# Optimization experiments

Hardware: AMD Instinct MI355X
Metric: run time of the kernel (lower is better)

The kernel has to match this reference:

```python
import jax, jax.numpy as jnp
import numpy as np
from jax.scipy.linalg import solve_triangular

B, T, HID = 1, 2048, 2048
HK, DK = 16, 96
HV, DV = 16, 192
KDIM, VDIM = HK * DK, HV * DV
KCONV = 4
CHUNK = 64
EPS = 1e-6


def setup_inputs():
    key = jax.random.key(0)
    ks = jax.random.split(key, 16)
    s = 0.02
    return {
        "hidden_states": jax.random.normal(ks[0], (B, T, HID), jnp.float32),
        "Wq": jax.random.normal(ks[1], (HID, KDIM), jnp.float32) * s,
        "Wk": jax.random.normal(ks[2], (HID, KDIM), jnp.float32) * s,
        "Wv": jax.random.normal(ks[3], (HID, VDIM), jnp.float32) * s,
        "Wb": jax.random.normal(ks[4], (HID, HV), jnp.float32) * s,
        "Wa": jax.random.normal(ks[5], (HID, HV), jnp.float32) * s,
        "Wg": jax.random.normal(ks[6], (HID, VDIM), jnp.float32) * s,
        "Wo": jax.random.normal(ks[7], (VDIM, HID), jnp.float32) * s,
        "conv_q": jax.random.normal(ks[8], (KDIM, KCONV), jnp.float32) * 0.5,
        "conv_k": jax.random.normal(ks[9], (KDIM, KCONV), jnp.float32) * 0.5,
        "conv_v": jax.random.normal(ks[10], (VDIM, KCONV), jnp.float32) * 0.5,
        "A_log": jnp.log(jax.random.uniform(ks[11], (HV,), jnp.float32, 1.0, 16.0)),
        "dt_bias": jax.random.uniform(ks[12], (HV,), jnp.float32, 0.0, 1.0),
        "norm_weight": jnp.ones((DV,), jnp.float32),
    }


def short_conv_silu(x, w):
    # x: [B,T,C], w: [C,K]; causal depthwise conv (left pad K-1) then SiLU
    K = w.shape[-1]
    xp = jnp.pad(x, ((0, 0), (K - 1, 0), (0, 0)))
    y = sum(xp[:, j:j + x.shape[1], :] * w[:, j] for j in range(K))
    return jax.nn.silu(y)


def l2norm(x):
    return x * jax.lax.rsqrt(jnp.sum(x * x, axis=-1, keepdims=True) + EPS)


def chunk_gated_delta_rule(q, k, v, g, beta):
    # q,k: [B,T,H,dk]; v: [B,T,H,dv]; g,beta: [B,T,H]. Chunked parallel scan (WY form).
    Bb, Tt, H, dk = q.shape
    dv = v.shape[-1]
    N = Tt // CHUNK
    q = l2norm(q) * (dk ** -0.5)
    k = l2norm(k)
    chunk = lambda x: x.transpose(0, 2, 1, 3).reshape(Bb, H, N, CHUNK, x.shape[-1])
    qc, kc, vc = chunk(q), chunk(k), chunk(v)
    gc = jnp.cumsum(g.transpose(0, 2, 1).reshape(Bb, H, N, CHUNK), axis=-1)
    bc = beta.transpose(0, 2, 1).reshape(Bb, H, N, CHUNK)

    m_inc = jnp.tril(jnp.ones((CHUNK, CHUNK), bool))
    m_str = jnp.tril(jnp.ones((CHUNK, CHUNK), bool), -1)
    diff = gc[..., :, None] - gc[..., None, :]
    D = jnp.exp(jnp.where(m_inc, diff, 0.0)) * m_inc  # [B,H,N,C,C] intra-chunk decay

    kb = kc * bc[..., None]
    A = -jnp.einsum('bhnik,bhnjk->bhnij', kb, kc) * D * m_str
    eye = jnp.eye(CHUNK, dtype=q.dtype)
    # UT transform: Tm = (I - A)^{-1}, A strictly lower triangular
    Tm = solve_triangular(eye - A, jnp.broadcast_to(eye, A.shape), lower=True, unit_diagonal=True)
    u = Tm @ (vc * bc[..., None])                   # [B,H,N,C,dv]
    w = Tm @ (kb * jnp.exp(gc)[..., None])          # [B,H,N,C,dk]
    g_last = gc[..., -1]                            # [B,H,N]

    def step(S, inp):
        q_i, k_i, u_i, w_i, g_i, D_i, gl = inp
        v_new = u_i - w_i @ S                       # [B,H,C,dv]
        attn = jnp.einsum('bhik,bhjk->bhij', q_i, k_i) * D_i
        o_i = (q_i * jnp.exp(g_i)[..., None]) @ S + attn @ v_new
        k_dec = k_i * jnp.exp(gl[..., None] - g_i)[..., None]
        S = S * jnp.exp(gl)[..., None, None] + jnp.einsum('bhck,bhcv->bhkv', k_dec, v_new)
        return S, o_i

    mv = lambda x: jnp.moveaxis(x, 2, 0)
    S0 = jnp.zeros((Bb, H, dk, dv), q.dtype)
    _, o = jax.lax.scan(step, S0, (mv(qc), mv(kc), mv(u), mv(w), mv(gc), mv(D), mv(g_last)))
    o = jnp.moveaxis(o, 0, 2).reshape(Bb, H, Tt, dv)
    return o.transpose(0, 2, 1, 3)                  # [B,T,H,dv]


def reference(hidden_states, Wq, Wk, Wv, Wb, Wa, Wg, Wo, conv_q, conv_k, conv_v, A_log, dt_bias, norm_weight):
    q = short_conv_silu(hidden_states @ Wq, conv_q).reshape(B, T, HK, DK)
    k = short_conv_silu(hidden_states @ Wk, conv_k).reshape(B, T, HK, DK)
    v = short_conv_silu(hidden_states @ Wv, conv_v).reshape(B, T, HV, DV)
    beta = jax.nn.sigmoid(hidden_states @ Wb) * 2.0          # allow_neg_eigval -> beta in [0,2]
    g = -jnp.exp(A_log) * jax.nn.softplus(hidden_states @ Wa + dt_bias)  # log decay, [B,T,HV]
    o = chunk_gated_delta_rule(q, k, v, g, beta)             # [B,T,HV,DV]
    gate = (hidden_states @ Wg).reshape(B, T, HV, DV)
    o = o * jax.nn.silu(gate)                                # gated RMSNorm (gate, then norm)
    o = o * jax.lax.rsqrt(jnp.mean(o * o, axis=-1, keepdims=True) + EPS) * norm_weight
    return o.reshape(B, T, VDIM) @ Wo
```

## Files before the change

kernel.cpp:

```cpp
#include <hip/hip_runtime.h>
#include <math.h>

#define T_LEN 2048
#define HIDN  2048
#define HKN   16
#define DKN   96
#define HVN   16
#define DVN   192
#define KDIMN 1536
#define VDIMN 3072
#define QKVD  6144
#define CHUNKN 64
#define NCHUNK 32
#define EPSF 1e-6f
#define TN_STRIDE 10240
#define WQG_ST 6656
#define AT_ST  4608
#define CT_ST  18432
#define S_ST   19968
#define U_ST   12288

typedef __attribute__((ext_vector_type(8))) short short8;
typedef __attribute__((ext_vector_type(4))) float f32x4;

__device__ __forceinline__ unsigned short f2bf(float f) {
    unsigned int u = __float_as_uint(f);
    unsigned int r = (u + 0x7FFFu + ((u >> 16) & 1u)) >> 16;
    return (unsigned short)r;
}
__device__ __forceinline__ float bf2f(unsigned short u) {
    return __uint_as_float(((unsigned int)u) << 16);
}
__device__ __forceinline__ float siluf(float x) { return x / (1.f + expf(-x)); }

__device__ __forceinline__ void gld_lds16(const void* g, void* l) {
    __builtin_amdgcn_global_load_lds((const __attribute__((address_space(1))) unsigned int*)g,
                                     (__attribute__((address_space(3))) unsigned int*)l, 16, 0, 0);
}

__global__ void prep_weights(const float* __restrict__ Wq, const float* __restrict__ Wk,
                             const float* __restrict__ Wv, const float* __restrict__ Wg,
                             const float* __restrict__ Wo,
                             unsigned short* __restrict__ WallT, unsigned short* __restrict__ WoT) {
    __shared__ float tile[64][65];
    int bid = blockIdx.x;
    const float* W; unsigned short* Wt; int K, N, l;
    if (bid < 768)       { W = Wq; Wt = WallT;                          K = 2048; N = 1536; l = bid; }
    else if (bid < 1536) { W = Wk; Wt = WallT + (size_t)1536 * 2048;    K = 2048; N = 1536; l = bid - 768; }
    else if (bid < 3072) { W = Wv; Wt = WallT + (size_t)3072 * 2048;    K = 2048; N = 3072; l = bid - 1536; }
    else if (bid < 4608) { W = Wg; Wt = WallT + (size_t)6144 * 2048;    K = 2048; N = 3072; l = bid - 3072; }
    else                 { W = Wo; Wt = WoT;                            K = 3072; N = 2048; l = bid - 4608; }
    int nbx = N >> 6;
    int n0 = (l % nbx) * 64, k0 = (l / nbx) * 64;
    int tx = threadIdx.x, ty = threadIdx.y;
    for (int r = ty; r < 64; r += 4) tile[r][tx] = W[(size_t)(k0 + r) * N + n0 + tx];
    __syncthreads();
    for (int r = ty; r < 64; r += 4) Wt[(size_t)(n0 + r) * K + k0 + tx] = f2bf(tile[tx][r]);
}

__global__ __launch_bounds__(256) void gemm_bt2(const unsigned short* __restrict__ A,
                                                const unsigned short* __restrict__ Bt,
                                                float* __restrict__ C1, int ld1, int nblk1,
                                                unsigned short* __restrict__ C2, int ld2,
                                                int M, int K) {
    __shared__ __align__(16) unsigned short As[2][128 * 32];
    __shared__ __align__(16) unsigned short Bs[2][128 * 32];
    int tid = threadIdx.x;
    int wave = tid >> 6, lane = tid & 63;
    int bm = blockIdx.y, bn = blockIdx.x;
    f32x4 acc[4][4] = {};
    int wr = wave >> 1, wc = wave & 1;
    int rstage = wave * 32 + (lane >> 2);
    int cstage = (lane & 3) * 8;
    const size_t a_row0 = (size_t)bm * 128;
    const size_t b_row0 = (size_t)bn * 128;
    const unsigned short* gaBase = A + (a_row0 + rstage) * (size_t)K + cstage;
    const unsigned short* gbBase = Bt + (b_row0 + rstage) * (size_t)K + cstage;
    int row_a[4], row_b[4];
#pragma unroll
    for (int i = 0; i < 4; ++i) {
        row_a[i] = wr * 64 + i * 16 + (lane & 15);
        row_b[i] = wc * 64 + i * 16 + (lane & 15);
    }
    int koff = (lane >> 4) * 8;
    int niter = K >> 5;
    {
        unsigned short* ab = &As[0][wave * 1024];
        unsigned short* bb = &Bs[0][wave * 1024];
        gld_lds16(gaBase, ab);
        gld_lds16(gaBase + (size_t)16 * K, ab + 512);
        gld_lds16(gbBase, bb);
        gld_lds16(gbBase + (size_t)16 * K, bb + 512);
    }
    __syncthreads();
    for (int i = 0; i < niter; ++i) {
        int cur = i & 1;
        if (i + 1 < niter) {
            int k0 = (i + 1) * 32;
            unsigned short* ab = &As[cur ^ 1][wave * 1024];
            unsigned short* bb = &Bs[cur ^ 1][wave * 1024];
            gld_lds16(gaBase + k0, ab);
            gld_lds16(gaBase + k0 + (size_t)16 * K, ab + 512);
            gld_lds16(gbBase + k0, bb);
            gld_lds16(gbBase + k0 + (size_t)16 * K, bb + 512);
        }
        short8 af[4], bfr[4];
#pragma unroll
        for (int mi = 0; mi < 4; ++mi) af[mi] = *(const short8*)&As[cur][row_a[mi] * 32 + koff];
#pragma unroll
        for (int ni = 0; ni < 4; ++ni) bfr[ni] = *(const short8*)&Bs[cur][row_b[ni] * 32 + koff];
#pragma unroll
        for (int mi = 0; mi < 4; ++mi)
#pragma unroll
            for (int ni = 0; ni < 4; ++ni)
                acc[mi][ni] = __builtin_amdgcn_mfma_f32_16x16x32_bf16(af[mi], bfr[ni], acc[mi][ni], 0, 0, 0);
        __syncthreads();
    }
    if (bn < nblk1) {
        int colb = bn * 128;
#pragma unroll
        for (int mi = 0; mi < 4; ++mi) {
            int rbase = bm * 128 + wr * 64 + mi * 16 + (lane >> 4) * 4;
#pragma unroll
            for (int ni = 0; ni < 4; ++ni) {
                int col = colb + wc * 64 + ni * 16 + (lane & 15);
#pragma unroll
                for (int j = 0; j < 4; ++j)
                    C1[(size_t)(rbase + j) * ld1 + col] = acc[mi][ni][j];
            }
        }
    } else {
        int colb = (bn - nblk1) * 128;
#pragma unroll
        for (int mi = 0; mi < 4; ++mi) {
            int rbase = bm * 128 + wr * 64 + mi * 16 + (lane >> 4) * 4;
#pragma unroll
            for (int ni = 0; ni < 4; ++ni) {
                int col = colb + wc * 64 + ni * 16 + (lane & 15);
#pragma unroll
                for (int j = 0; j < 4; ++j)
                    C2[(size_t)(rbase + j) * ld2 + col] = f2bf(acc[mi][ni][j]);
            }
        }
    }
}

__global__ __launch_bounds__(256) void gemm_btk(const unsigned short* __restrict__ A,
                                                const unsigned short* __restrict__ Bt,
                                                float* __restrict__ C, float* __restrict__ Cp,
                                                int M, int N, int K) {
    __shared__ __align__(16) unsigned short As[2][128 * 32];
    __shared__ __align__(16) unsigned short Bs[2][128 * 32];
    int tid = threadIdx.x;
    int wave = tid >> 6, lane = tid & 63;
    int bm = blockIdx.y, bn = blockIdx.x, kz = blockIdx.z;
    int kchunk = K / 3;
    int kbeg = kz * kchunk;
    f32x4 acc[4][4] = {};
    int wr = wave >> 1, wc = wave & 1;
    int rstage = wave * 32 + (lane >> 2);
    int cstage = (lane & 3) * 8;
    const size_t a_row0 = (size_t)bm * 128;
    const size_t b_row0 = (size_t)bn * 128;
    const unsigned short* gaBase = A + (a_row0 + rstage) * (size_t)K + kbeg + cstage;
    const unsigned short* gbBase = Bt + (b_row0 + rstage) * (size_t)K + kbeg + cstage;
    int row_a[4], row_b[4];
#pragma unroll
    for (int i = 0; i < 4; ++i) {
        row_a[i] = wr * 64 + i * 16 + (lane & 15);
        row_b[i] = wc * 64 + i * 16 + (lane & 15);
    }
    int koff = (lane >> 4) * 8;
    int niter = kchunk >> 5;
    {
        unsigned short* ab = &As[0][wave * 1024];
        unsigned short* bb = &Bs[0][wave * 1024];
        gld_lds16(gaBase, ab);
        gld_lds16(gaBase + (size_t)16 * K, ab + 512);
        gld_lds16(gbBase, bb);
        gld_lds16(gbBase + (size_t)16 * K, bb + 512);
    }
    __syncthreads();
    for (int i = 0; i < niter; ++i) {
        int cur = i & 1;
        if (i + 1 < niter) {
            int k0 = (i + 1) * 32;
            unsigned short* ab = &As[cur ^ 1][wave * 1024];
            unsigned short* bb = &Bs[cur ^ 1][wave * 1024];
            gld_lds16(gaBase + k0, ab);
            gld_lds16(gaBase + k0 + (size_t)16 * K, ab + 512);
            gld_lds16(gbBase + k0, bb);
            gld_lds16(gbBase + k0 + (size_t)16 * K, bb + 512);
        }
        short8 af[4], bfr[4];
#pragma unroll
        for (int mi = 0; mi < 4; ++mi) af[mi] = *(const short8*)&As[cur][row_a[mi] * 32 + koff];
#pragma unroll
        for (int ni = 0; ni < 4; ++ni) bfr[ni] = *(const short8*)&Bs[cur][row_b[ni] * 32 + koff];
#pragma unroll
        for (int mi = 0; mi < 4; ++mi)
#pragma unroll
            for (int ni = 0; ni < 4; ++ni)
                acc[mi][ni] = __builtin_amdgcn_mfma_f32_16x16x32_bf16(af[mi], bfr[ni], acc[mi][ni], 0, 0, 0);
        __syncthreads();
    }
    float* Cout = (kz == 0) ? C : (Cp + (size_t)(kz - 1) * M * N);
#pragma unroll
    for (int mi = 0; mi < 4; ++mi) {
        int rbase = bm * 128 + wr * 64 + mi * 16 + (lane >> 4) * 4;
#pragma unroll
        for (int ni = 0; ni < 4; ++ni) {
            int col = bn * 128 + wc * 64 + ni * 16 + (lane & 15);
#pragma unroll
            for (int j = 0; j < 4; ++j)
                Cout[(size_t)(rbase + j) * N + col] = acc[mi][ni][j];
        }
    }
}

__global__ void addk(float* __restrict__ out, const float* __restrict__ p, int n) {
    int i = (blockIdx.x * blockDim.x + threadIdx.x) * 4;
    if (i >= n) return;
    float4 a = *(const float4*)(out + i);
    float4 b = *(const float4*)(p + i);
    float4 c = *(const float4*)(p + n + i);
    a.x += b.x + c.x; a.y += b.y + c.y; a.z += b.z + c.z; a.w += b.w + c.w;
    *(float4*)(out + i) = a;
}

__global__ __launch_bounds__(256) void beta_g(const float* __restrict__ X,
                                              const float* __restrict__ Wb, const float* __restrict__ Wa,
                                              const float* __restrict__ A_log, const float* __restrict__ dtb,
                                              float* __restrict__ bvec, float* __restrict__ gvec,
                                              unsigned short* __restrict__ Xbf) {
    int t = blockIdx.x;
    int tid = threadIdx.x;
    int cg = tid & 7, ks = tid >> 3;
    int wave = tid >> 6, lane = tid & 63;
    const float* xr = X + (size_t)t * HIDN;
    const float* Wsel = (cg < 4) ? Wb : Wa;
    int cc = (cg & 3) * 4;
    float ax = 0.f, ay = 0.f, az = 0.f, aw = 0.f;
#pragma unroll 4
    for (int i = 0; i < 16; ++i) {
        int k = (ks + 32 * i) * 4;
        float4 xv = *(const float4*)(xr + k);
        if (cg == 0) {
            ushort4 xo;
            xo.x = f2bf(xv.x); xo.y = f2bf(xv.y); xo.z = f2bf(xv.z); xo.w = f2bf(xv.w);
            *(ushort4*)(Xbf + (size_t)t * HIDN + k) = xo;
        }
        float4 w0 = *(const float4*)(Wsel + (size_t)(k + 0) * 16 + cc);
        float4 w1 = *(const float4*)(Wsel + (size_t)(k + 1) * 16 + cc);
        float4 w2 = *(const float4*)(Wsel + (size_t)(k + 2) * 16 + cc);
        float4 w3 = *(const float4*)(Wsel + (size_t)(k + 3) * 16 + cc);
        ax += xv.x * w0.x + xv.y * w1.x + xv.z * w2.x + xv.w * w3.x;
        ay += xv.x * w0.y + xv.y * w1.y + xv.z * w2.y + xv.w * w3.y;
        az += xv.x * w0.z + xv.y * w1.z + xv.z * w2.z + xv.w * w3.z;
        aw += xv.x * w0.w + xv.y * w1.w + xv.z * w2.w + xv.w * w3.w;
    }
#pragma unroll
    for (int off = 8; off <= 32; off <<= 1) {
        ax += __shfl_xor(ax, off, 64);
        ay += __shfl_xor(ay, off, 64);
        az += __shfl_xor(az, off, 64);
        aw += __shfl_xor(aw, off, 64);
    }
    __shared__ float red[4][8][4];
    if ((lane >> 3) == 0) {
        red[wave][cg][0] = ax; red[wave][cg][1] = ay;
        red[wave][cg][2] = az; red[wave][cg][3] = aw;
    }
    __syncthreads();
    if (tid < 8) {
        float tot[4];
#pragma unroll
        for (int j = 0; j < 4; ++j)
            tot[j] = red[0][tid][j] + red[1][tid][j] + red[2][tid][j] + red[3][tid][j];
        int c0 = (tid & 3) * 4;
        if (tid < 4) {
#pragma unroll
            for (int j = 0; j < 4; ++j)
                bvec[(size_t)t * 16 + c0 + j] = 2.f / (1.f + expf(-tot[j]));
        } else {
#pragma unroll
            for (int j = 0; j < 4; ++j) {
                float a = tot[j] + dtb[c0 + j];
                float sp = (a > 20.f) ? a : log1pf(expf(a));
                gvec[(size_t)t * 16 + c0 + j] = -expf(A_log[c0 + j]) * sp;
            }
        }
    }
}

__global__ __launch_bounds__(256) void phase1_mfma(
    const float* __restrict__ Cqkv,
    const float* __restrict__ cq, const float* __restrict__ ck, const float* __restrict__ cv,
    const float* __restrict__ gvec, const float* __restrict__ bvec,
    float* __restrict__ u_ws, unsigned short* __restrict__ w_bf,
    unsigned short* __restrict__ qg_bf, unsigned short* __restrict__ at_bf,
    unsigned short* __restrict__ Ct, unsigned short* __restrict__ Tn) {
    int n = blockIdx.x, h = blockIdx.y;
    int t0 = n * CHUNKN;
    int tid = threadIdx.x;
    int wave = tid >> 6, lane = tid & 63;
    size_t base = (size_t)(h * NCHUNK + n);

    __shared__ __align__(16) char LB1[139776];
    unsigned short* QKb  = (unsigned short*)(LB1 + 0);
    unsigned short* Pb   = (unsigned short*)(LB1 + 26624);
    unsigned short* RHSw = (unsigned short*)(LB1 + 39936);
    unsigned short* RHSv = (unsigned short*)(LB1 + 53760);
    unsigned short* Ab   = (unsigned short*)(LB1 + 81408);
    unsigned short* Atb  = (unsigned short*)(LB1 + 94720);
    unsigned short* Ptb  = (unsigned short*)(LB1 + 108032);
    float*          Pf   = (float*)(LB1 + 121344);
    unsigned short* kdT  = (unsigned short*)(LB1 + 81408);
    unsigned short* wT   = (unsigned short*)(LB1 + 95232);
    unsigned short* uT   = (unsigned short*)(LB1 + 109056);
    float* gr_s = (float*)(LB1 + 138752);
    float* gc_s = gr_s + 64;
    float* be_s = gc_s + 64;
    float* egc  = be_s + 64;
    __shared__ __align__(16) float cwS[384 * 4];

    for (int f = tid; f < 384; f += 256) {
        const float* src = (f < 96)  ? (cq + (size_t)(h * 96 + f) * 4)
                         : (f < 192) ? (ck + (size_t)(h * 96 + f - 96) * 4)
                                     : (cv + (size_t)(h * 192 + f - 192) * 4);
        *(float4*)&cwS[f * 4] = *(const float4*)src;
    }
    if (tid < 64) {
        gr_s[tid] = gvec[(size_t)(t0 + tid) * HVN + h];
        be_s[tid] = bvec[(size_t)(t0 + tid) * HVN + h];
    }
    __syncthreads();
    if (tid < 64) {
        float sacc = 0.f;
        for (int j = 0; j <= tid; ++j) sacc += gr_s[j];
        gc_s[tid] = sacc;
    }
    __syncthreads();
    float gl = gc_s[63];
    if (tid < 64) egc[tid] = expf(gl - gc_s[tid]);

    int r = tid >> 2, sub = tid & 3;
    int trow = t0 + r;
    {
        int gc0 = 1536 + h * DKN + sub * 24;
        int lc0 = 96 + sub * 24;
        float kreg[24];
        float ss = 0.f;
#pragma unroll
        for (int i = 0; i < 6; ++i) {
            float4 x0 = (trow >= 3) ? *(const float4*)(Cqkv + (size_t)(trow - 3) * QKVD + gc0 + i * 4) : make_float4(0, 0, 0, 0);
            float4 x1 = (trow >= 2) ? *(const float4*)(Cqkv + (size_t)(trow - 2) * QKVD + gc0 + i * 4) : make_float4(0, 0, 0, 0);
            float4 x2 = (trow >= 1) ? *(const float4*)(Cqkv + (size_t)(trow - 1) * QKVD + gc0 + i * 4) : make_float4(0, 0, 0, 0);
            float4 x3 = *(const float4*)(Cqkv + (size_t)trow * QKVD + gc0 + i * 4);
#pragma unroll
            for (int c = 0; c < 4; ++c) {
                float4 w = *(const float4*)&cwS[(lc0 + i * 4 + c) * 4];
                float xv = ((const float*)&x0)[c] * w.x + ((const float*)&x1)[c] * w.y
                         + ((const float*)&x2)[c] * w.z + ((const float*)&x3)[c] * w.w;
                xv = siluf(xv);
                kreg[i * 4 + c] = xv;
                ss += xv * xv;
            }
        }
        ss += __shfl_xor(ss, 1, 64);
        ss += __shfl_xor(ss, 2, 64);
        float nrm = rsqrtf(ss + EPSF);
        float ebg = be_s[r] * expf(gc_s[r]);
#pragma unroll
        for (int i = 0; i < 24; ++i) {
            float kn = kreg[i] * nrm;
            QKb[r * 104 + sub * 24 + i] = f2bf(kn);
            RHSw[(sub * 24 + i) * 72 + r] = f2bf(kn * ebg);
        }
    }
    {
        int gc0 = h * DKN + sub * 24;
        int lc0 = sub * 24;
        float qreg[24];
        float ss = 0.f;
#pragma unroll
        for (int i = 0; i < 6; ++i) {
            float4 x0 = (trow >= 3) ? *(const float4*)(Cqkv + (size_t)(trow - 3) * QKVD + gc0 + i * 4) : make_float4(0, 0, 0, 0);
            float4 x1 = (trow >= 2) ? *(const float4*)(Cqkv + (size_t)(trow - 2) * QKVD + gc0 + i * 4) : make_float4(0, 0, 0, 0);
            float4 x2 = (trow >= 1) ? *(const float4*)(Cqkv + (size_t)(trow - 1) * QKVD + gc0 + i * 4) : make_float4(0, 0, 0, 0);
            float4 x3 = *(const float4*)(Cqkv + (size_t)trow * QKVD + gc0 + i * 4);
#pragma unroll
            for (int c = 0; c < 4; ++c) {
                float4 w = *(const float4*)&cwS[(lc0 + i * 4 + c) * 4];
                float xv = ((const float*)&x0)[c] * w.x + ((const float*)&x1)[c] * w.y
                         + ((const float*)&x2)[c] * w.z + ((const float*)&x3)[c] * w.w;
                xv = siluf(xv);
                qreg[i * 4 + c] = xv;
                ss += xv * xv;
            }
        }
        ss += __shfl_xor(ss, 1, 64);
        ss += __shfl_xor(ss, 2, 64);
        float nrm = rsqrtf(ss + EPSF) * 0.10206207261596577f;
        float eg = expf(gc_s[r]);
        unsigned short* qgp = qg_bf + base * WQG_ST + r * 104 + sub * 24;
#pragma unroll
        for (int i = 0; i < 24; ++i) {
            float qn = qreg[i] * nrm;
            QKb[(64 + r) * 104 + sub * 24 + i] = f2bf(qn);
            qgp[i] = f2bf(qn * eg);
        }
    }
    {
        int gc0 = 3072 + h * DVN + sub * 48;
        int lc0 = 192 + sub * 48;
        float ber = be_s[r];
#pragma unroll
        for (int i = 0; i < 12; ++i) {
            float4 x0 = (trow >= 3) ? *(const float4*)(Cqkv + (size_t)(trow - 3) * QKVD + gc0 + i * 4) : make_float4(0, 0, 0, 0);
            float4 x1 = (trow >= 2) ? *(const float4*)(Cqkv + (size_t)(trow - 2) * QKVD + gc0 + i * 4) : make_float4(0, 0, 0, 0);
            float4 x2 = (trow >= 1) ? *(const float4*)(Cqkv + (size_t)(trow - 1) * QKVD + gc0 + i * 4) : make_float4(0, 0, 0, 0);
            float4 x3 = *(const float4*)(Cqkv + (size_t)trow * QKVD + gc0 + i * 4);
#pragma unroll
            for (int c = 0; c < 4; ++c) {
                float4 w = *(const float4*)&cwS[(lc0 + i * 4 + c) * 4];
                float xv = ((const float*)&x0)[c] * w.x + ((const float*)&x1)[c] * w.y
                         + ((const float*)&x2)[c] * w.z + ((const float*)&x3)[c] * w.w;
                RHSv[(sub * 48 + i * 4 + c) * 72 + r] = f2bf(siluf(xv) * ber);
            }
        }
    }
    __syncthreads();

    {
        f32x4 acc1[2][4] = {};
#pragma unroll
        for (int ks = 0; ks < 3; ++ks) {
            int ko = ks * 32 + (lane >> 4) * 8;
            short8 af[2], bfv[4];
#pragma unroll
            for (int rt2 = 0; rt2 < 2; ++rt2)
                af[rt2] = *(const short8*)&QKb[(wave * 32 + rt2 * 16 + (lane & 15)) * 104 + ko];
#pragma unroll
            for (int ct = 0; ct < 4; ++ct)
                bfv[ct] = *(const short8*)&QKb[(ct * 16 + (lane & 15)) * 104 + ko];
#pragma unroll
            for (int rt2 = 0; rt2 < 2; ++rt2)
#pragma unroll
                for (int ct = 0; ct < 4; ++ct)
                    acc1[rt2][ct] = __builtin_amdgcn_mfma_f32_16x16x32_bf16(af[rt2], bfv[ct], acc1[rt2][ct], 0, 0, 0);
        }
#pragma unroll
        for (int rt2 = 0; rt2 < 2; ++rt2)
#pragma unroll
            for (int ct = 0; ct < 4; ++ct)
#pragma unroll
                for (int j = 0; j < 4; ++j) {
                    int rr = wave * 32 + rt2 * 16 + (lane >> 4) * 4 + j;
                    int cc = ct * 16 + (lane & 15);
                    float val = acc1[rt2][ct][j];
                    if (rr < 64) {
                        float av = (rr > cc) ? -be_s[rr] * expf(gc_s[rr] - gc_s[cc]) * val : 0.f;
                        unsigned short ab = f2bf(av);
                        Ab[rr * 104 + cc] = ab;
                        Atb[cc * 104 + rr] = ab;
                        float pv = (rr == cc) ? 1.f : av;
                        Pf[rr * 68 + cc] = pv;
                        unsigned short pb = f2bf(pv);
                        Pb[rr * 104 + cc] = pb;
                        Ptb[cc * 104 + rr] = pb;
                    } else {
                        int ar = rr - 64;
                        float av = (ar >= cc) ? expf(gc_s[ar] - gc_s[cc]) * val : 0.f;
                        at_bf[base * AT_ST + ar * 72 + cc] = f2bf(av);
                    }
                }
    }
    __syncthreads();

#pragma unroll 1
    for (int lev = 0; lev < 5; ++lev) {
        f32x4 d[4] = {};
#pragma unroll
        for (int ks = 0; ks < 2; ++ks) {
            int ko = ks * 32 + (lane >> 4) * 8;
            short8 a0 = *(const short8*)&Ab[(wave * 16 + (lane & 15)) * 104 + ko];
#pragma unroll
            for (int ct = 0; ct < 4; ++ct) {
                short8 b0 = *(const short8*)&Atb[(ct * 16 + (lane & 15)) * 104 + ko];
                d[ct] = __builtin_amdgcn_mfma_f32_16x16x32_bf16(a0, b0, d[ct], 0, 0, 0);
            }
        }
        __syncthreads();
#pragma unroll
        for (int ct = 0; ct < 4; ++ct)
#pragma unroll
            for (int j = 0; j < 4; ++j) {
                int rr = wave * 16 + (lane >> 4) * 4 + j;
                int cc = ct * 16 + (lane & 15);
                unsigned short hb = f2bf(d[ct][j]);
                Ab[rr * 104 + cc] = hb;
                Atb[cc * 104 + rr] = hb;
            }
        __syncthreads();
        f32x4 e[4];
#pragma unroll
        for (int ct = 0; ct < 4; ++ct)
#pragma unroll
            for (int j = 0; j < 4; ++j)
                e[ct][j] = Pf[(wave * 16 + (lane >> 4) * 4 + j) * 68 + ct * 16 + (lane & 15)];
#pragma unroll
        for (int ks = 0; ks < 2; ++ks) {
            int ko = ks * 32 + (lane >> 4) * 8;
            short8 a0 = *(const short8*)&Ab[(wave * 16 + (lane & 15)) * 104 + ko];
#pragma unroll
            for (int ct = 0; ct < 4; ++ct) {
                short8 b0 = *(const short8*)&Ptb[(ct * 16 + (lane & 15)) * 104 + ko];
                e[ct] = __builtin_amdgcn_mfma_f32_16x16x32_bf16(a0, b0, e[ct], 0, 0, 0);
            }
        }
        __syncthreads();
#pragma unroll
        for (int ct = 0; ct < 4; ++ct)
#pragma unroll
            for (int j = 0; j < 4; ++j) {
                int rr = wave * 16 + (lane >> 4) * 4 + j;
                int cc = ct * 16 + (lane & 15);
                float pv = e[ct][j];
                Pf[rr * 68 + cc] = pv;
                unsigned short pb = f2bf(pv);
                Pb[rr * 104 + cc] = pb;
                Ptb[cc * 104 + rr] = pb;
            }
        __syncthreads();
    }
    for (int f = tid; f < 6144; f += 256) {
        int d = f >> 6, tt = f & 63;
        kdT[d * 72 + tt] = f2bf(bf2f(QKb[tt * 104 + d]) * egc[tt]);
    }

#pragma unroll 1
    for (int i = 0; i < 18; ++i) {
        int id = wave * 18 + i;
        int rt = id & 3, ct = id >> 2;
        f32x4 o4 = {};
#pragma unroll
        for (int ks = 0; ks < 2; ++ks) {
            int ko = ks * 32 + (lane >> 4) * 8;
            short8 a0 = *(const short8*)&Pb[(rt * 16 + (lane & 15)) * 104 + ko];
            short8 b0 = (ct < 12)
                ? *(const short8*)&RHSv[(ct * 16 + (lane & 15)) * 72 + ko]
                : *(const short8*)&RHSw[((ct - 12) * 16 + (lane & 15)) * 72 + ko];
            o4 = __builtin_amdgcn_mfma_f32_16x16x32_bf16(a0, b0, o4, 0, 0, 0);
        }
#pragma unroll
        for (int j = 0; j < 4; ++j) {
            int rr = rt * 16 + (lane >> 4) * 4 + j;
            int nn = ct * 16 + (lane & 15);
            if (ct < 12) {
                u_ws[base * U_ST + rr * 192 + nn] = o4[j];
                uT[nn * 72 + rr] = f2bf(o4[j]);
            } else {
                w_bf[base * WQG_ST + rr * 104 + (nn - 192)] = f2bf(-o4[j]);
                wT[(nn - 192) * 72 + rr] = f2bf(o4[j]);
            }
        }
    }
    __syncthreads();

    float eglv = expf(gl);
#pragma unroll 1
    for (int q = 0; q < 27; ++q) {
        int id = wave * 27 + q;
        f32x4 acc = {};
        if (id < 36) {
            int jt = id / 6, kt = id % 6;
#pragma unroll
            for (int ks = 0; ks < 2; ++ks) {
                int ko = ks * 32 + (lane >> 4) * 8;
                short8 a0 = *(const short8*)&kdT[(jt * 16 + (lane & 15)) * 72 + ko];
                short8 b0 = *(const short8*)&wT[(kt * 16 + (lane & 15)) * 72 + ko];
                acc = __builtin_amdgcn_mfma_f32_16x16x32_bf16(a0, b0, acc, 0, 0, 0);
            }
#pragma unroll
            for (int rr = 0; rr < 4; ++rr) {
                int j = jt * 16 + (lane >> 4) * 4 + rr;
                int k = kt * 16 + (lane & 15);
                float val = -acc[rr];
                if (j == k) val += eglv;
                Tn[base * TN_STRIDE + j * 104 + k] = f2bf(val);
            }
        } else {
            int cid = id - 36;
            int it = cid / 6, jt = cid % 6;
#pragma unroll
            for (int ks = 0; ks < 2; ++ks) {
                int ko = ks * 32 + (lane >> 4) * 8;
                short8 a0 = *(const short8*)&uT[(it * 16 + (lane & 15)) * 72 + ko];
                short8 b0 = *(const short8*)&kdT[(jt * 16 + (lane & 15)) * 72 + ko];
                acc = __builtin_amdgcn_mfma_f32_16x16x32_bf16(a0, b0, acc, 0, 0, 0);
            }
#pragma unroll
            for (int rr = 0; rr < 4; ++rr)
                Ct[base * CT_ST + (size_t)(it * 16 + (lane >> 4) * 4 + rr) * 96 + jt * 16 + (lane & 15)] = f2bf(acc[rr]);
        }
    }
}

__global__ __launch_bounds__(128) void mscan(const unsigned short* __restrict__ Ct,
                                             const unsigned short* __restrict__ Tn,
                                             unsigned short* __restrict__ s_bf) {
    int rg = blockIdx.x, h = blockIdx.y;
    int tid = threadIdx.x, wave = tid >> 6, lane = tid & 63;
    __shared__ __align__(16) unsigned short St[48 * 104];
    __shared__ __align__(16) unsigned short TnB[2][TN_STRIDE];
    __shared__ __align__(16) unsigned short CtB[2][48 * 96];
    for (int i = tid; i < 48 * 104; i += 128) St[i] = 0;

    {
        const char* cp = (const char*)(Ct + (size_t)(h * NCHUNK) * CT_ST + rg * (48 * 96));
        const char* tp = (const char*)(Tn + (size_t)(h * NCHUNK) * TN_STRIDE);
        for (int q = wave; q < 9; q += 2)
            gld_lds16(cp + (size_t)q * 1024 + lane * 16, (char*)&CtB[0][0] + (size_t)q * 1024);
#pragma unroll
        for (int q = 0; q < 10; ++q) {
            size_t o = (size_t)(wave * 10 + q) * 1024 + lane * 16;
            gld_lds16(tp + o, (char*)&TnB[0][0] + (size_t)(wave * 10 + q) * 1024);
        }
    }
    f32x4 acc[3][3];
    int colw = wave * 48;
    __syncthreads();

#pragma unroll 1
    for (int n = 0; n < NCHUNK; ++n) {
        size_t base = (size_t)(h * NCHUNK + n);
        int cur = n & 1;
        if (n + 1 < NCHUNK) {
            const char* cp = (const char*)(Ct + (base + 1) * CT_ST + rg * (48 * 96));
            const char* tp = (const char*)(Tn + (base + 1) * TN_STRIDE);
            for (int q = wave; q < 9; q += 2)
                gld_lds16(cp + (size_t)q * 1024 + lane * 16, (char*)&CtB[cur ^ 1][0] + (size_t)q * 1024);
#pragma unroll
            for (int q = 0; q < 10; ++q) {
                size_t o = (size_t)(wave * 10 + q) * 1024 + lane * 16;
                gld_lds16(tp + o, (char*)&TnB[cur ^ 1][0] + (size_t)(wave * 10 + q) * 1024);
            }
        }
        {
            unsigned short* sp = s_bf + base * S_ST + rg * 4992;
            for (int f = tid; f < 624; f += 128)
                *(short8*)(sp + f * 8) = *(const short8*)&St[f * 8];
        }
#pragma unroll
        for (int it = 0; it < 3; ++it)
#pragma unroll
            for (int jt = 0; jt < 3; ++jt) {
                int irow = it * 16 + (lane >> 4) * 4;
                int col = colw + jt * 16 + (lane & 15);
#pragma unroll
                for (int r = 0; r < 4; ++r)
                    acc[it][jt][r] = bf2f(CtB[cur][(irow + r) * 96 + col]);
            }
#pragma unroll
        for (int ks = 0; ks < 3; ++ks) {
            int ko = ks * 32 + (lane >> 4) * 8;
            short8 af[3], bfv[3];
#pragma unroll
            for (int it = 0; it < 3; ++it)
                af[it] = *(const short8*)&St[(it * 16 + (lane & 15)) * 104 + ko];
#pragma unroll
            for (int jt = 0; jt < 3; ++jt)
                bfv[jt] = *(const short8*)&TnB[cur][(colw + jt * 16 + (lane & 15)) * 104 + ko];
#pragma unroll
            for (int it = 0; it < 3; ++it)
#pragma unroll
                for (int jt = 0; jt < 3; ++jt)
                    acc[it][jt] = __builtin_amdgcn_mfma_f32_16x16x32_bf16(af[it], bfv[jt], acc[it][jt], 0, 0, 0);
        }
        __syncthreads();
#pragma unroll
        for (int it = 0; it < 3; ++it)
#pragma unroll
            for (int jt = 0; jt < 3; ++jt)
#pragma unroll
                for (int r = 0; r < 4; ++r)
                    St[(it * 16 + (lane >> 4) * 4 + r) * 104 + colw + jt * 16 + (lane & 15)] = f2bf(acc[it][jt][r]);
        __syncthreads();
    }
}

#define P2_ST 0
#define P2_W  39936
#define P2_QG 53248
#define P2_AT 66560
#define P2_U  75776
#define P2_VN 125952
__global__ __launch_bounds__(256) void phase2b_mfma(const unsigned short* __restrict__ s_bf,
                                                    const unsigned short* __restrict__ w_bf,
                                                    const unsigned short* __restrict__ qg_bf,
                                                    const unsigned short* __restrict__ at_bf,
                                                    const float* __restrict__ u_ws,
                                                    const unsigned short* __restrict__ Cgate,
                                                    const float* __restrict__ nw,
                                                    unsigned short* __restrict__ obf) {
    __shared__ __align__(16) char LB[153600];
    unsigned short* StB = (unsigned short*)(LB + P2_ST);
    unsigned short* wB  = (unsigned short*)(LB + P2_W);
    unsigned short* qgB = (unsigned short*)(LB + P2_QG);
    unsigned short* atB = (unsigned short*)(LB + P2_AT);
    float* uF           = (float*)(LB + P2_U);
    unsigned short* vnB = (unsigned short*)(LB + P2_VN);
    int n = blockIdx.x, h = blockIdx.y;
    size_t base = (size_t)(h * NCHUNK + n);
    int tid = threadIdx.x, wave = tid >> 6, lane = tid & 63;
    int i0w = wave * 48;
    {
        const char* sp = (const char*)(s_bf + base * S_ST);
        const char* wp = (const char*)(w_bf + base * WQG_ST);
        const char* qp = (const char*)(qg_bf + base * WQG_ST);
        const char* ap = (const char*)(at_bf + base * AT_ST);
        for (int q = wave; q < 39; q += 4)
            gld_lds16(sp + (size_t)q * 1024 + lane * 16, LB + P2_ST + (size_t)q * 1024);
        for (int q = wave; q < 13; q += 4)
            gld_lds16(wp + (size_t)q * 1024 + lane * 16, LB + P2_W + (size_t)q * 1024);
        for (int q = wave; q < 13; q += 4)
            gld_lds16(qp + (size_t)q * 1024 + lane * 16, LB + P2_QG + (size_t)q * 1024);
        for (int q = wave; q < 9; q += 4)
            gld_lds16(ap + (size_t)q * 1024 + lane * 16, LB + P2_AT + (size_t)q * 1024);
    }
    {
        const float* up = u_ws + base * U_ST;
        for (int f = tid; f < 3072; f += 256) {
            int t = f / 48, c4 = (f % 48) * 4;
            *(float4*)&uF[t * 196 + c4] = *(const float4*)(up + t * 192 + c4);
        }
    }
    __syncthreads();
    {
        f32x4 acc[3][4];
#pragma unroll
        for (int it = 0; it < 3; ++it)
#pragma unroll
            for (int jt = 0; jt < 4; ++jt)
#pragma unroll
                for (int r = 0; r < 4; ++r)
                    acc[it][jt][r] = uF[(jt * 16 + (lane & 15)) * 196 + i0w + it * 16 + (lane >> 4) * 4 + r];
#pragma unroll
        for (int ks = 0; ks < 3; ++ks) {
            int ko = ks * 32 + (lane >> 4) * 8;
            short8 af[3], bfv[4];
#pragma unroll
            for (int it = 0; it < 3; ++it)
                af[it] = *(const short8*)&StB[(i0w + it * 16 + (lane & 15)) * 104 + ko];
#pragma unroll
            for (int jt = 0; jt < 4; ++jt)
                bfv[jt] = *(const short8*)&wB[(jt * 16 + (lane & 15)) * 104 + ko];
#pragma unroll
            for (int it = 0; it < 3; ++it)
#pragma unroll
                for (int jt = 0; jt < 4; ++jt)
                    acc[it][jt] = __builtin_amdgcn_mfma_f32_16x16x32_bf16(af[it], bfv[jt], acc[it][jt], 0, 0, 0);
        }
#pragma unroll
        for (int it = 0; it < 3; ++it)
#pragma unroll
            for (int jt = 0; jt < 4; ++jt)
#pragma unroll
                for (int r = 0; r < 4; ++r)
                    vnB[(i0w + it * 16 + (lane >> 4) * 4 + r) * 72 + jt * 16 + (lane & 15)] = f2bf(acc[it][jt][r]);
    }
    f32x4 acc2[3][4] = {};
#pragma unroll
    for (int ks = 0; ks < 3; ++ks) {
        int ko = ks * 32 + (lane >> 4) * 8;
        short8 af[3], bfv[4];
#pragma unroll
        for (int it = 0; it < 3; ++it)
            af[it] = *(const short8*)&StB[(i0w + it * 16 + (lane & 15)) * 104 + ko];
#pragma unroll
        for (int jt = 0; jt < 4; ++jt)
            bfv[jt] = *(const short8*)&qgB[(jt * 16 + (lane & 15)) * 104 + ko];
#pragma unroll
        for (int it = 0; it < 3; ++it)
#pragma unroll
            for (int jt = 0; jt < 4; ++jt)
                acc2[it][jt] = __builtin_amdgcn_mfma_f32_16x16x32_bf16(af[it], bfv[jt], acc2[it][jt], 0, 0, 0);
    }
#pragma unroll
    for (int ks = 0; ks < 2; ++ks) {
        int ko = ks * 32 + (lane >> 4) * 8;
        short8 af[3], bfv[4];
#pragma unroll
        for (int it = 0; it < 3; ++it)
            af[it] = *(const short8*)&vnB[(i0w + it * 16 + (lane & 15)) * 72 + ko];
#pragma unroll
        for (int jt = 0; jt < 4; ++jt)
            bfv[jt] = *(const short8*)&atB[(jt * 16 + (lane & 15)) * 72 + ko];
#pragma unroll
        for (int it = 0; it < 3; ++it)
#pragma unroll
            for (int jt = 0; jt < 4; ++jt)
                acc2[it][jt] = __builtin_amdgcn_mfma_f32_16x16x32_bf16(af[it], bfv[jt], acc2[it][jt], 0, 0, 0);
    }
    __syncthreads();
    float* oF = (float*)(LB + 0);
#pragma unroll
    for (int it = 0; it < 3; ++it)
#pragma unroll
        for (int jt = 0; jt < 4; ++jt)
#pragma unroll
            for (int r = 0; r < 4; ++r)
                oF[(i0w + it * 16 + (lane >> 4) * 4 + r) * 68 + jt * 16 + (lane & 15)] = acc2[it][jt][r];
    __syncthreads();

    float* ssq = (float*)(LB + 131072);
    float* rno = (float*)(LB + 132096);
    int jj = tid >> 2, qq = tid & 3;
    int t0 = n * CHUNKN;
    {
        const unsigned short* gp = Cgate + (size_t)(t0 + jj) * VDIMN + h * DVN + qq * 48;
        float ss = 0.f;
#pragma unroll 4
        for (int m = 0; m < 48; ++m) {
            int i = qq * 48 + m;
            float x = oF[i * 68 + jj];
            float g = bf2f(gp[m]);
            float xv = x * siluf(g);
            oF[i * 68 + jj] = xv;
            ss += xv * xv;
        }
        ssq[jj * 4 + qq] = ss;
    }
    __syncthreads();
    if (tid < 64) {
        float tot = ssq[tid * 4] + ssq[tid * 4 + 1] + ssq[tid * 4 + 2] + ssq[tid * 4 + 3];
        rno[tid] = rsqrtf(tot * (1.f / 192.f) + EPSF);
    }
    __syncthreads();
    {
        float rr2 = rno[jj];
        unsigned short* op = obf + (size_t)(t0 + jj) * VDIMN + h * DVN + qq * 48;
#pragma unroll 4
        for (int m = 0; m < 48; ++m) {
            int i = qq * 48 + m;
            op[m] = f2bf(oF[i * 68 + jj] * rr2 * nw[i]);
        }
    }
}

extern "C" void kernel_launch(void* const* d_in, const int* in_sizes, int n_in,
                              void* d_out, int out_size, void* d_ws, size_t ws_size,
                              hipStream_t stream) {
    (void)in_sizes; (void)n_in; (void)out_size;
    const float* X    = (const float*)d_in[0];
    const float* Wq   = (const float*)d_in[1];
    const float* Wk   = (const float*)d_in[2];
    const float* Wv   = (const float*)d_in[3];
    const float* Wb   = (const float*)d_in[4];
    const float* Wa   = (const float*)d_in[5];
    const float* Wg   = (const float*)d_in[6];
    const float* Wo   = (const float*)d_in[7];
    const float* cq   = (const float*)d_in[8];
    const float* ck   = (const float*)d_in[9];
    const float* cv   = (const float*)d_in[10];
    const float* Alog = (const float*)d_in[11];
    const float* dtb  = (const float*)d_in[12];
    const float* nw   = (const float*)d_in[13];

    const size_t OFF_XBF   = 0;
    const size_t OFF_WALLT = 8388608;
    const size_t OFF_WOT   = 46137344;
    const size_t OFF_CQKV  = 58720256;
    const size_t OFF_CGATE = 109051904;
    const size_t OFF_CT    = 134217728;
    const size_t OFF_TN    = OFF_CT + 37748736;
    const size_t OFF_GVEC  = 184549376;
    const size_t OFF_BVEC  = 184680448;
    const size_t OFF_U     = 184819712;
    const size_t OFF_W     = 209985536;
    const size_t OFF_QG    = 222568448;
    const size_t OFF_AT    = OFF_XBF;
    const size_t OFF_S     = OFF_CQKV;
    const size_t OFF_OBF   = OFF_WALLT + 25165824;
    const size_t OFF_OPART = OFF_CQKV;
    const size_t NEEDED    = 235151360;
    if (ws_size < NEEDED) return;

    char* ws = (char*)d_ws;
    unsigned short* Xbf   = (unsigned short*)(ws + OFF_XBF);
    unsigned short* WallT = (unsigned short*)(ws + OFF_WALLT);
    unsigned short* WoT   = (unsigned short*)(ws + OFF_WOT);
    float* Cqkv  = (float*)(ws + OFF_CQKV);
    unsigned short* Cgate = (unsigned short*)(ws + OFF_CGATE);
    float* gvec  = (float*)(ws + OFF_GVEC);
    float* bvec  = (float*)(ws + OFF_BVEC);
    float* u_ws  = (float*)(ws + OFF_U);
    unsigned short* w_bf  = (unsigned short*)(ws + OFF_W);
    unsigned short* qg_bf = (unsigned short*)(ws + OFF_QG);
    unsigned short* at_bf = (unsigned short*)(ws + OFF_AT);
    unsigned short* Ct    = (unsigned short*)(ws + OFF_CT);
    unsigned short* Tn    = (unsigned short*)(ws + OFF_TN);
    unsigned short* s_bf  = (unsigned short*)(ws + OFF_S);
    unsigned short* obf   = (unsigned short*)(ws + OFF_OBF);
    float* opart = (float*)(ws + OFF_OPART);

    beta_g<<<T_LEN, 256, 0, stream>>>(X, Wb, Wa, Alog, dtb, bvec, gvec, Xbf);
    prep_weights<<<6144, dim3(64, 4), 0, stream>>>(Wq, Wk, Wv, Wg, Wo, WallT, WoT);

    gemm_bt2<<<dim3(9216 / 128, 2048 / 128), 256, 0, stream>>>(Xbf, WallT,
                                                               Cqkv, QKVD, QKVD / 128,
                                                               Cgate, VDIMN, 2048, 2048);

    phase1_mfma<<<dim3(NCHUNK, HVN), 256, 0, stream>>>(Cqkv, cq, ck, cv, gvec, bvec,
                                                       u_ws, w_bf, qg_bf, at_bf, Ct, Tn);
    mscan<<<dim3(4, HVN), 128, 0, stream>>>(Ct, Tn, s_bf);
    phase2b_mfma<<<dim3(NCHUNK, HVN), 256, 0, stream>>>(s_bf, w_bf, qg_bf, at_bf, u_ws,
                                                        Cgate, nw, obf);

    gemm_btk<<<dim3(2048 / 128, 2048 / 128, 3), 256, 0, stream>>>(obf, WoT, (float*)d_out, opart,
                                                                  2048, 2048, 3072);
    addk<<<4096, 256, 0, stream>>>((float*)d_out, opart, 2048 * 2048);
}
```

Before: 402.7 us.

## Merge prep kernels and restructure triangular inverse doubling to one sync phase per level

Fuses the beta/g projection kernel and the weight transpose/convert kernel into one launch, removing a kernel launch boundary. In phase1, the product-form inverse (I+A)(I+A^2)... is rewritten so that each level computes both the next power of A and the accumulated product P from the same operands in one pass. This removes one barrier pair and the transposed P buffer per level, at the cost of one extra level of the product MMA. The merged prep kernel shares an LDS footprint and launch config between two different workloads.

```diff
diff --git a/kernel.cpp b/kernel.cpp
--- a/kernel.cpp
+++ b/kernel.cpp
@@ -38,24 +38,91 @@
                                      (__attribute__((address_space(3))) unsigned int*)l, 16, 0, 0);
 }
 
-__global__ void prep_weights(const float* __restrict__ Wq, const float* __restrict__ Wk,
-                             const float* __restrict__ Wv, const float* __restrict__ Wg,
-                             const float* __restrict__ Wo,
-                             unsigned short* __restrict__ WallT, unsigned short* __restrict__ WoT) {
+__global__ __launch_bounds__(256) void prep_all(
+    const float* __restrict__ X,
+    const float* __restrict__ Wb, const float* __restrict__ Wa,
+    const float* __restrict__ A_log, const float* __restrict__ dtb,
+    float* __restrict__ bvec, float* __restrict__ gvec, unsigned short* __restrict__ Xbf,
+    const float* __restrict__ Wq, const float* __restrict__ Wk,
+    const float* __restrict__ Wv, const float* __restrict__ Wg,
+    const float* __restrict__ Wo,
+    unsigned short* __restrict__ WallT, unsigned short* __restrict__ WoT) {
     __shared__ float tile[64][65];
+    __shared__ float red[4][8][4];
     int bid = blockIdx.x;
-    const float* W; unsigned short* Wt; int K, N, l;
-    if (bid < 768)       { W = Wq; Wt = WallT;                          K = 2048; N = 1536; l = bid; }
-    else if (bid < 1536) { W = Wk; Wt = WallT + (size_t)1536 * 2048;    K = 2048; N = 1536; l = bid - 768; }
-    else if (bid < 3072) { W = Wv; Wt = WallT + (size_t)3072 * 2048;    K = 2048; N = 3072; l = bid - 1536; }
-    else if (bid < 4608) { W = Wg; Wt = WallT + (size_t)6144 * 2048;    K = 2048; N = 3072; l = bid - 3072; }
-    else                 { W = Wo; Wt = WoT;                            K = 3072; N = 2048; l = bid - 4608; }
-    int nbx = N >> 6;
-    int n0 = (l % nbx) * 64, k0 = (l / nbx) * 64;
-    int tx = threadIdx.x, ty = threadIdx.y;
-    for (int r = ty; r < 64; r += 4) tile[r][tx] = W[(size_t)(k0 + r) * N + n0 + tx];
-    __syncthreads();
-    for (int r = ty; r < 64; r += 4) Wt[(size_t)(n0 + r) * K + k0 + tx] = f2bf(tile[tx][r]);
+    int tid = threadIdx.x;
+    if (bid < 2048) {
+        int t = bid;
+        int cg = tid & 7, ks = tid >> 3;
+        int wave = tid >> 6, lane = tid & 63;
+        const float* xr = X + (size_t)t * HIDN;
+        const float* Wsel = (cg < 4) ? Wb : Wa;
+        int cc = (cg & 3) * 4;
+        float ax = 0.f, ay = 0.f, az = 0.f, aw = 0.f;
+#pragma unroll 4
+        for (int i = 0; i < 16; ++i) {
+            int k = (ks + 32 * i) * 4;
+            float4 xv = *(const float4*)(xr + k);
+            if (cg == 0) {
+                ushort4 xo;
+                xo.x = f2bf(xv.x); xo.y = f2bf(xv.y); xo.z = f2bf(xv.z); xo.w = f2bf(xv.w);
+                *(ushort4*)(Xbf + (size_t)t * HIDN + k) = xo;
+            }
+            float4 w0 = *(const float4*)(Wsel + (size_t)(k + 0) * 16 + cc);
+            float4 w1 = *(const float4*)(Wsel + (size_t)(k + 1) * 16 + cc);
+            float4 w2 = *(const float4*)(Wsel + (size_t)(k + 2) * 16 + cc);
+            float4 w3 = *(const float4*)(Wsel + (size_t)(k + 3) * 16 + cc);
+            ax += xv.x * w0.x + xv.y * w1.x + xv.z * w2.x + xv.w * w3.x;
+            ay += xv.x * w0.y + xv.y * w1.y + xv.z * w2.y + xv.w * w3.y;
+            az += xv.x * w0.z + xv.y * w1.z + xv.z * w2.z + xv.w * w3.z;
+            aw += xv.x * w0.w + xv.y * w1.w + xv.z * w2.w + xv.w * w3.w;
+        }
+#pragma unroll
+        for (int off = 8; off <= 32; off <<= 1) {
+            ax += __shfl_xor(ax, off, 64);
+            ay += __shfl_xor(ay, off, 64);
+            az += __shfl_xor(az, off, 64);
+            aw += __shfl_xor(aw, off, 64);
+        }
+        if ((lane >> 3) == 0) {
+            red[wave][cg][0] = ax; red[wave][cg][1] = ay;
+            red[wave][cg][2] = az; red[wave][cg][3] = aw;
+        }
+        __syncthreads();
+        if (tid < 8) {
+            float tot[4];
+#pragma unroll
+            for (int j = 0; j < 4; ++j)
+                tot[j] = red[0][tid][j] + red[1][tid][j] + red[2][tid][j] + red[3][tid][j];
+            int c0 = (tid & 3) * 4;
+            if (tid < 4) {
+#pragma unroll
+                for (int j = 0; j < 4; ++j)
+                    bvec[(size_t)t * 16 + c0 + j] = 2.f / (1.f + expf(-tot[j]));
+            } else {
+#pragma unroll
+                for (int j = 0; j < 4; ++j) {
+                    float a = tot[j] + dtb[c0 + j];
+                    float sp = (a > 20.f) ? a : log1pf(expf(a));
+                    gvec[(size_t)t * 16 + c0 + j] = -expf(A_log[c0 + j]) * sp;
+                }
+            }
+        }
+    } else {
+        int b2 = bid - 2048;
+        const float* W; unsigned short* Wt; int K, N, l;
+        if (b2 < 768)       { W = Wq; Wt = WallT;                       K = 2048; N = 1536; l = b2; }
+        else if (b2 < 1536) { W = Wk; Wt = WallT + (size_t)1536 * 2048; K = 2048; N = 1536; l = b2 - 768; }
+        else if (b2 < 3072) { W = Wv; Wt = WallT + (size_t)3072 * 2048; K = 2048; N = 3072; l = b2 - 1536; }
+        else if (b2 < 4608) { W = Wg; Wt = WallT + (size_t)6144 * 2048; K = 2048; N = 3072; l = b2 - 3072; }
+        else                { W = Wo; Wt = WoT;                         K = 3072; N = 2048; l = b2 - 4608; }
+        int nbx = N >> 6;
+        int n0 = (l % nbx) * 64, k0 = (l / nbx) * 64;
+        int tx = tid & 63, ty = tid >> 6;
+        for (int r = ty; r < 64; r += 4) tile[r][tx] = W[(size_t)(k0 + r) * N + n0 + tx];
+        __syncthreads();
+        for (int r = ty; r < 64; r += 4) Wt[(size_t)(n0 + r) * K + k0 + tx] = f2bf(tile[tx][r]);
+    }
 }
 
 __global__ __launch_bounds__(256) void gemm_bt2(const unsigned short* __restrict__ A,
@@ -228,71 +295,6 @@
     *(float4*)(out + i) = a;
 }
 
-__global__ __launch_bounds__(256) void beta_g(const float* __restrict__ X,
-                                              const float* __restrict__ Wb, const float* __restrict__ Wa,
-                                              const float* __restrict__ A_log, const float* __restrict__ dtb,
-                                              float* __restrict__ bvec, float* __restrict__ gvec,
-                                              unsigned short* __restrict__ Xbf) {
-    int t = blockIdx.x;
-    int tid = threadIdx.x;
-    int cg = tid & 7, ks = tid >> 3;
-    int wave = tid >> 6, lane = tid & 63;
-    const float* xr = X + (size_t)t * HIDN;
-    const float* Wsel = (cg < 4) ? Wb : Wa;
-    int cc = (cg & 3) * 4;
-    float ax = 0.f, ay = 0.f, az = 0.f, aw = 0.f;
-#pragma unroll 4
-    for (int i = 0; i < 16; ++i) {
-        int k = (ks + 32 * i) * 4;
-        float4 xv = *(const float4*)(xr + k);
-        if (cg == 0) {
-            ushort4 xo;
-            xo.x = f2bf(xv.x); xo.y = f2bf(xv.y); xo.z = f2bf(xv.z); xo.w = f2bf(xv.w);
-            *(ushort4*)(Xbf + (size_t)t * HIDN + k) = xo;
-        }
-        float4 w0 = *(const float4*)(Wsel + (size_t)(k + 0) * 16 + cc);
-        float4 w1 = *(const float4*)(Wsel + (size_t)(k + 1) * 16 + cc);
-        float4 w2 = *(const float4*)(Wsel + (size_t)(k + 2) * 16 + cc);
-        float4 w3 = *(const float4*)(Wsel + (size_t)(k + 3) * 16 + cc);
-        ax += xv.x * w0.x + xv.y * w1.x + xv.z * w2.x + xv.w * w3.x;
-        ay += xv.x * w0.y + xv.y * w1.y + xv.z * w2.y + xv.w * w3.y;
-        az += xv.x * w0.z + xv.y * w1.z + xv.z * w2.z + xv.w * w3.z;
-        aw += xv.x * w0.w + xv.y * w1.w + xv.z * w2.w + xv.w * w3.w;
-    }
-#pragma unroll
-    for (int off = 8; off <= 32; off <<= 1) {
-        ax += __shfl_xor(ax, off, 64);
-        ay += __shfl_xor(ay, off, 64);
-        az += __shfl_xor(az, off, 64);
-        aw += __shfl_xor(aw, off, 64);
-    }
-    __shared__ float red[4][8][4];
-    if ((lane >> 3) == 0) {
-        red[wave][cg][0] = ax; red[wave][cg][1] = ay;
-        red[wave][cg][2] = az; red[wave][cg][3] = aw;
-    }
-    __syncthreads();
-    if (tid < 8) {
-        float tot[4];
-#pragma unroll
-        for (int j = 0; j < 4; ++j)
-            tot[j] = red[0][tid][j] + red[1][tid][j] + red[2][tid][j] + red[3][tid][j];
-        int c0 = (tid & 3) * 4;
-        if (tid < 4) {
-#pragma unroll
-            for (int j = 0; j < 4; ++j)
-                bvec[(size_t)t * 16 + c0 + j] = 2.f / (1.f + expf(-tot[j]));
-        } else {
-#pragma unroll
-            for (int j = 0; j < 4; ++j) {
-                float a = tot[j] + dtb[c0 + j];
-                float sp = (a > 20.f) ? a : log1pf(expf(a));
-                gvec[(size_t)t * 16 + c0 + j] = -expf(A_log[c0 + j]) * sp;
-            }
-        }
-    }
-}
-
 __global__ __launch_bounds__(256) void phase1_mfma(
     const float* __restrict__ Cqkv,
     const float* __restrict__ cq, const float* __restrict__ ck, const float* __restrict__ cv,
@@ -313,7 +315,6 @@
     unsigned short* RHSv = (unsigned short*)(LB1 + 53760);
     unsigned short* Ab   = (unsigned short*)(LB1 + 81408);
     unsigned short* Atb  = (unsigned short*)(LB1 + 94720);
-    unsigned short* Ptb  = (unsigned short*)(LB1 + 108032);
     float*          Pf   = (float*)(LB1 + 121344);
     unsigned short* kdT  = (unsigned short*)(LB1 + 81408);
     unsigned short* wT   = (unsigned short*)(LB1 + 95232);
@@ -464,11 +465,9 @@
                         unsigned short ab = f2bf(av);
                         Ab[rr * 104 + cc] = ab;
                         Atb[cc * 104 + rr] = ab;
-                        float pv = (rr == cc) ? 1.f : av;
+                        float pv = (rr == cc) ? 1.f : 0.f;
                         Pf[rr * 68 + cc] = pv;
-                        unsigned short pb = f2bf(pv);
-                        Pb[rr * 104 + cc] = pb;
-                        Ptb[cc * 104 + rr] = pb;
+                        Pb[rr * 104 + cc] = f2bf(pv);
                     } else {
                         int ar = rr - 64;
                         float av = (ar >= cc) ? expf(gc_s[ar] - gc_s[cc]) * val : 0.f;
@@ -479,16 +478,24 @@
     __syncthreads();
 
 #pragma unroll 1
-    for (int lev = 0; lev < 5; ++lev) {
+    for (int lev = 0; lev < 6; ++lev) {
         f32x4 d[4] = {};
+        f32x4 e[4];
+#pragma unroll
+        for (int ct = 0; ct < 4; ++ct)
+#pragma unroll
+            for (int j = 0; j < 4; ++j)
+                e[ct][j] = Pf[(wave * 16 + (lane >> 4) * 4 + j) * 68 + ct * 16 + (lane & 15)];
 #pragma unroll
         for (int ks = 0; ks < 2; ++ks) {
             int ko = ks * 32 + (lane >> 4) * 8;
-            short8 a0 = *(const short8*)&Ab[(wave * 16 + (lane & 15)) * 104 + ko];
+            short8 aA = *(const short8*)&Ab[(wave * 16 + (lane & 15)) * 104 + ko];
+            short8 aP = *(const short8*)&Pb[(wave * 16 + (lane & 15)) * 104 + ko];
 #pragma unroll
             for (int ct = 0; ct < 4; ++ct) {
-                short8 b0 = *(const short8*)&Atb[(ct * 16 + (lane & 15)) * 104 + ko];
-                d[ct] = __builtin_amdgcn_mfma_f32_16x16x32_bf16(a0, b0, d[ct], 0, 0, 0);
+                short8 bAt = *(const short8*)&Atb[(ct * 16 + (lane & 15)) * 104 + ko];
+                if (lev < 5) d[ct] = __builtin_amdgcn_mfma_f32_16x16x32_bf16(aA, bAt, d[ct], 0, 0, 0);
+                e[ct] = __builtin_amdgcn_mfma_f32_16x16x32_bf16(aP, bAt, e[ct], 0, 0, 0);
             }
         }
         __syncthreads();
@@ -498,39 +505,14 @@
             for (int j = 0; j < 4; ++j) {
                 int rr = wave * 16 + (lane >> 4) * 4 + j;
                 int cc = ct * 16 + (lane & 15);
-                unsigned short hb = f2bf(d[ct][j]);
-                Ab[rr * 104 + cc] = hb;
-                Atb[cc * 104 + rr] = hb;
-            }
-        __syncthreads();
-        f32x4 e[4];
-#pragma unroll
-        for (int ct = 0; ct < 4; ++ct)
-#pragma unroll
-            for (int j = 0; j < 4; ++j)
-                e[ct][j] = Pf[(wave * 16 + (lane >> 4) * 4 + j) * 68 + ct * 16 + (lane & 15)];
-#pragma unroll
-        for (int ks = 0; ks < 2; ++ks) {
-            int ko = ks * 32 + (lane >> 4) * 8;
-            short8 a0 = *(const short8*)&Ab[(wave * 16 + (lane & 15)) * 104 + ko];
-#pragma unroll
-            for (int ct = 0; ct < 4; ++ct) {
-                short8 b0 = *(const short8*)&Ptb[(ct * 16 + (lane & 15)) * 104 + ko];
-                e[ct] = __builtin_amdgcn_mfma_f32_16x16x32_bf16(a0, b0, e[ct], 0, 0, 0);
-            }
-        }
-        __syncthreads();
-#pragma unroll
-        for (int ct = 0; ct < 4; ++ct)
-#pragma unroll
-            for (int j = 0; j < 4; ++j) {
-                int rr = wave * 16 + (lane >> 4) * 4 + j;
-                int cc = ct * 16 + (lane & 15);
+                if (lev < 5) {
+                    unsigned short hb = f2bf(d[ct][j]);
+                    Ab[rr * 104 + cc] = hb;
+                    Atb[cc * 104 + rr] = hb;
+                }
                 float pv = e[ct][j];
                 Pf[rr * 68 + cc] = pv;
-                unsigned short pb = f2bf(pv);
-                Pb[rr * 104 + cc] = pb;
-                Ptb[cc * 104 + rr] = pb;
+                Pb[rr * 104 + cc] = f2bf(pv);
             }
         __syncthreads();
     }
@@ -905,8 +887,8 @@
     unsigned short* obf   = (unsigned short*)(ws + OFF_OBF);
     float* opart = (float*)(ws + OFF_OPART);
 
-    beta_g<<<T_LEN, 256, 0, stream>>>(X, Wb, Wa, Alog, dtb, bvec, gvec, Xbf);
-    prep_weights<<<6144, dim3(64, 4), 0, stream>>>(Wq, Wk, Wv, Wg, Wo, WallT, WoT);
+    prep_all<<<8192, 256, 0, stream>>>(X, Wb, Wa, Alog, dtb, bvec, gvec, Xbf,
+                                       Wq, Wk, Wv, Wg, Wo, WallT, WoT);
 
     gemm_bt2<<<dim3(9216 / 128, 2048 / 128), 256, 0, stream>>>(Xbf, WallT,
                                                                Cqkv, QKVD, QKVD / 128,
```

New measurement: 400.8 us. About the same (-0.5%).
